# Kernel tuning notes

Hardware: AMD Instinct MI355X
Metric: run time of the kernel (lower is better)

Reference implementation:

```python
import jax, jax.numpy as jnp
import numpy as np

N, D, H, DH, FF, NE, NNZ = 4096, 128, 2, 64, 256, 2048, 65536
EPS = 1e-5

def layer_norm(x, g, b):
    m = jnp.mean(x, axis=-1, keepdims=True)
    v = jnp.var(x, axis=-1, keepdims=True)
    return (x - m) / jnp.sqrt(v + EPS) * g + b

def setup_inputs() -> dict:
    key = jax.random.key(0)
    ks = jax.random.split(key, 24)
    s = 0.05
    node_idx = jax.random.randint(ks[1], (NNZ,), 0, N)
    he_idx = jax.random.randint(ks[2], (NNZ,), 0, NE)
    return {
        "x": jax.random.normal(ks[0], (N, D), dtype=jnp.float32),
        "edge": jnp.stack([node_idx, he_idx]).astype(jnp.int64),
        "Wq": jax.random.normal(ks[3], (D, D)) * s, "bq": jnp.zeros((D,)),
        "Wk": jax.random.normal(ks[4], (D, D)) * s, "bk": jnp.zeros((D,)),
        "Wv": jax.random.normal(ks[5], (D, D)) * s, "bv": jnp.zeros((D,)),
        "Wo": jax.random.normal(ks[6], (D, D)) * s, "bo": jnp.zeros((D,)),
        "g_ln1": jnp.ones((D,)), "b_ln1": jnp.zeros((D,)),
        "W1": jax.random.normal(ks[7], (D, FF)) * s, "bf1": jnp.zeros((FF,)),
        "W2": jax.random.normal(ks[8], (FF, D)) * s, "bf2": jnp.zeros((D,)),
        "g_ln2": jnp.ones((D,)), "b_ln2": jnp.zeros((D,)),
        "Wh": jax.random.normal(ks[9], (D, D)) * s, "bh": jnp.zeros((D,)),
    }

def reference(x, edge, Wq, bq, Wk, bk, Wv, bv, Wo, bo, g_ln1, b_ln1,
              W1, bf1, W2, bf2, g_ln2, b_ln2, Wh, bh):
    # dropout layers run in eval mode (identity) for a deterministic reference
    def mha_block(h):
        q = (h @ Wq + bq).reshape(N, H, DH)
        k = (h @ Wk + bk).reshape(N, H, DH)
        v = (h @ Wv + bv).reshape(N, H, DH)
        scores = jnp.einsum('nhd,mhd->hnm', q, k) / jnp.sqrt(jnp.float32(DH))
        attn = jax.nn.softmax(scores, axis=-1)            # [H,N,N]
        o = jnp.einsum('hnm,mhd->nhd', attn, v).reshape(N, D)
        return layer_norm(h + o @ Wo + bo, g_ln1, b_ln1)

    def ff_block(h):
        z = jax.nn.sigmoid(h @ W1 + bf1)
        return layer_norm(h + z @ W2 + bf2, g_ln2, b_ln2)

    h = ff_block(mha_block(x))
    h = ff_block(mha_block(h))

    # HypergraphConv: out = D^{-1} H B^{-1} H^T (X Theta) + bias
    node_idx = edge[0]
    he_idx = edge[1]
    xt = h @ Wh                                            # [N,D]
    ones = jnp.ones((NNZ,), dtype=xt.dtype)
    Bdeg = jax.ops.segment_sum(ones, he_idx, num_segments=NE)
    Binv = jnp.where(Bdeg > 0, 1.0 / Bdeg, 0.0)
    Ddeg = jax.ops.segment_sum(ones, node_idx, num_segments=N)
    Dinv = jnp.where(Ddeg > 0, 1.0 / Ddeg, 0.0)
    e = jax.ops.segment_sum(xt[node_idx], he_idx, num_segments=NE) * Binv[:, None]
    out = jax.ops.segment_sum(e[he_idx], node_idx, num_segments=N) * Dinv[:, None] + bh
    return jax.nn.relu(out)
```

## Files before the change

### kernel.cpp

```cpp
#include <hip/hip_runtime.h>
#include <hip/hip_bf16.h>
#include <cstddef>

#define N_NODES 4096
#define DIM     128
#define NHEAD   2
#define DHEAD   64
#define FFDIM   256
#define NEDGE   2048
#define NNZ_E   65536
#define NSPLIT  8

typedef __attribute__((ext_vector_type(8))) short bf16x8;
typedef __attribute__((ext_vector_type(4))) float f32x4;
typedef unsigned short u16;

__device__ __forceinline__ u16 f2b(float f) {
    unsigned u = __float_as_uint(f);
    return (u16)((u + 0x7FFFu + ((u >> 16) & 1u)) >> 16);
}
__device__ __forceinline__ float b2f_bits(u16 h) {
    return __uint_as_float(((unsigned)h) << 16);
}

__global__ void prep(const float* __restrict__ x, float* __restrict__ h,
                     u16* __restrict__ hh, u16* __restrict__ hl,
                     const float* W0, const float* W1, const float* W2,
                     const float* W3, const float* W4, const float* W5,
                     const float* W6,
                     u16* P0, u16* P1, u16* P2, u16* P3, u16* P4, u16* P5, u16* P6,
                     int* __restrict__ cnt) {
    const int bx = blockIdx.x;
    if (bx < 2048) {
        int i = bx * 256 + threadIdx.x;
        float f = x[i];
        h[i] = f;
        u16 hi = f2b(f);
        hh[i] = hi;
        hl[i] = f2b(f - b2f_bits(hi));
        return;
    }
    if (bx >= 2944) {
        int i = (bx - 2944) * 256 + threadIdx.x;
        if (i < NEDGE + N_NODES) cnt[i] = 0;
        return;
    }
    const int p = bx - 2048;
    const int sel = p >> 7;
    const float* W; u16* P; int K, NC;
    switch (sel) {
        case 0: W = W0; P = P0; K = 128; NC = 128; break;
        case 1: W = W1; P = P1; K = 128; NC = 128; break;
        case 2: W = W2; P = P2; K = 128; NC = 128; break;
        case 3: W = W3; P = P3; K = 128; NC = 128; break;
        case 4: W = W4; P = P4; K = 128; NC = 128; break;
        case 5: W = W5; P = P5; K = 128; NC = 256; break;
        default: W = W6; P = P6; K = 256; NC = 128; break;
    }
    int i = (p & 127) * 256 + threadIdx.x;
    if (i < K * NC) {
        int k = i / NC, n = i % NC;
        float f = W[i];
        u16 hb = f2b(f);
        size_t o = ((size_t)(k >> 3) * NC + n) * 8 + (k & 7);
        P[o] = hb;
        P[(size_t)K * NC + o] = f2b(f - b2f_bits(hb));
    }
}

template<int K, int NC>
__global__ __launch_bounds__(256) void gemm_mfma(const u16* __restrict__ Ah,
                                                 const u16* __restrict__ Al,
                                                 const u16* __restrict__ Wp,
                                                 float* __restrict__ C0) {
    const int tid = threadIdx.x, w = tid >> 6, lane = tid & 63;
    const int qi = lane & 15, gi = lane >> 4;
    const int row0 = blockIdx.x * 64 + w * 16;
    const int col0 = blockIdx.y * 32;
    const u16* Wlo = Wp + (size_t)K * NC;

    f32x4 acc[2];
    acc[0] = (f32x4){0.f, 0.f, 0.f, 0.f};
    acc[1] = (f32x4){0.f, 0.f, 0.f, 0.f};

#pragma unroll 4
    for (int kc = 0; kc < K / 32; ++kc) {
        const int k0 = kc * 32;
        const size_t ao = (size_t)(row0 + qi) * K + k0 + gi * 8;
        bf16x8 ah = *(const bf16x8*)(Ah + ao);
        bf16x8 al = *(const bf16x8*)(Al + ao);
#pragma unroll
        for (int c = 0; c < 2; ++c) {
            const size_t wo = ((size_t)(k0 / 8 + gi) * NC + col0 + c * 16 + qi) * 8;
            bf16x8 wh = *(const bf16x8*)(Wp + wo);
            bf16x8 wl = *(const bf16x8*)(Wlo + wo);
            acc[c] = __builtin_amdgcn_mfma_f32_16x16x32_bf16(ah, wh, acc[c], 0, 0, 0);
            acc[c] = __builtin_amdgcn_mfma_f32_16x16x32_bf16(al, wh, acc[c], 0, 0, 0);
            acc[c] = __builtin_amdgcn_mfma_f32_16x16x32_bf16(ah, wl, acc[c], 0, 0, 0);
        }
    }

#pragma unroll
    for (int c = 0; c < 2; ++c) {
        const int col = col0 + c * 16 + qi;
#pragma unroll
        for (int r = 0; r < 4; ++r) {
            const int grow = row0 + gi * 4 + r;
            C0[(size_t)grow * NC + col] = acc[c][r];
        }
    }
}

__global__ __launch_bounds__(256) void qkv_mfma(const u16* __restrict__ Ah,
                                                const u16* __restrict__ Al,
                                                const u16* __restrict__ Wq,
                                                const u16* __restrict__ Wk,
                                                const u16* __restrict__ Wv,
                                                const float* __restrict__ bq,
                                                const float* __restrict__ bk,
                                                const float* __restrict__ bv,
                                                u16* __restrict__ qb,
                                                u16* __restrict__ kb,
                                                u16* __restrict__ vtb) {
    const int K = 128, NC = 128;
    const int tid = threadIdx.x, w = tid >> 6, lane = tid & 63;
    const int qi = lane & 15, gi = lane >> 4;
    const int row0 = blockIdx.x * 64 + w * 16;
    const int sel = blockIdx.y >> 2;
    const int col0 = (blockIdx.y & 3) * 32;
    const u16* Wp = (sel == 0) ? Wq : (sel == 1) ? Wk : Wv;
    const float* bias = (sel == 0) ? bq : (sel == 1) ? bk : bv;
    const u16* Wlo = Wp + (size_t)K * NC;

    f32x4 acc[2];
    acc[0] = (f32x4){0.f, 0.f, 0.f, 0.f};
    acc[1] = (f32x4){0.f, 0.f, 0.f, 0.f};

#pragma unroll 4
    for (int kc = 0; kc < K / 32; ++kc) {
        const int k0 = kc * 32;
        const size_t ao = (size_t)(row0 + qi) * K + k0 + gi * 8;
        bf16x8 ah = *(const bf16x8*)(Ah + ao);
        bf16x8 al = *(const bf16x8*)(Al + ao);
#pragma unroll
        for (int c = 0; c < 2; ++c) {
            const size_t wo = ((size_t)(k0 / 8 + gi) * NC + col0 + c * 16 + qi) * 8;
            bf16x8 wh = *(const bf16x8*)(Wp + wo);
            bf16x8 wl = *(const bf16x8*)(Wlo + wo);
            acc[c] = __builtin_amdgcn_mfma_f32_16x16x32_bf16(ah, wh, acc[c], 0, 0, 0);
            acc[c] = __builtin_amdgcn_mfma_f32_16x16x32_bf16(al, wh, acc[c], 0, 0, 0);
            acc[c] = __builtin_amdgcn_mfma_f32_16x16x32_bf16(ah, wl, acc[c], 0, 0, 0);
        }
    }

#pragma unroll
    for (int c = 0; c < 2; ++c) {
        const int col = col0 + c * 16 + qi;
        const int hh = col >> 6, d = col & 63;
        float bv_ = bias[col];
        if (sel < 2) {
            u16* dst = (sel == 0) ? qb : kb;
#pragma unroll
            for (int r = 0; r < 4; ++r) {
                const int grow = row0 + gi * 4 + r;
                dst[((size_t)hh * N_NODES + grow) * 64 + d] = f2b(acc[c][r] + bv_);
            }
        } else {
            const int grow0 = row0 + gi * 4;
            ushort4 pw;
            pw.x = f2b(acc[c][0] + bv_);
            pw.y = f2b(acc[c][1] + bv_);
            pw.z = f2b(acc[c][2] + bv_);
            pw.w = f2b(acc[c][3] + bv_);
            *(ushort4*)&vtb[((size_t)hh * 64 + d) * N_NODES + grow0] = pw;
        }
    }
}

#define ROWP 72
__global__ __launch_bounds__(256) void attn_mfma(const u16* __restrict__ qb,
                                                 const u16* __restrict__ kb,
                                                 const u16* __restrict__ vtb,
                                                 float* __restrict__ op,
                                                 float* __restrict__ mlm,
                                                 float* __restrict__ mll) {
    __shared__ __align__(16) u16 k_s[64 * ROWP];
    __shared__ __align__(16) u16 vt_s[64 * ROWP];
    __shared__ __align__(16) u16 p_s[4][16 * ROWP];
    const int h = blockIdx.y;
    const int s = blockIdx.z;
    const int row0 = blockIdx.x * 64;
    const int tid = threadIdx.x;
    const int w = tid >> 6, lane = tid & 63;
    const int qi = lane & 15, gi = lane >> 4;
    const float CE = 0.18033688011f;

    const u16* qrow = qb + ((size_t)h * N_NODES + row0 + w * 16 + qi) * 64 + gi * 8;
    bf16x8 qf0 = *(const bf16x8*)qrow;
    bf16x8 qf1 = *(const bf16x8*)(qrow + 32);

    f32x4 oc[4];
#pragma unroll
    for (int i = 0; i < 4; ++i) oc[i] = (f32x4){0.f, 0.f, 0.f, 0.f};
    float m_run = -INFINITY, l_run = 0.f;

    const u16* kbh = kb + (size_t)h * N_NODES * 64;
    const u16* vth = vtb + (size_t)h * 64 * N_NODES;

    for (int kt = s * (N_NODES / 64 / NSPLIT); kt < (s + 1) * (N_NODES / 64 / NSPLIT); ++kt) {
        const u16* ksrc = kbh + kt * 64 * 64;
#pragma unroll
        for (int i = 0; i < 2; ++i) {
            int c = tid + i * 256;
            int r = c >> 3, ss = c & 7;
            *(uint4*)&k_s[r * ROWP + ss * 8]  = *(const uint4*)(ksrc + c * 8);
            *(uint4*)&vt_s[r * ROWP + ss * 8] = *(const uint4*)(vth + (size_t)r * N_NODES + kt * 64 + ss * 8);
        }
        __syncthreads();

        f32x4 sc[4];
#pragma unroll
        for (int t = 0; t < 4; ++t) {
            const u16* krow = &k_s[(t * 16 + qi) * ROWP + gi * 8];
            bf16x8 ka0 = *(const bf16x8*)krow;
            bf16x8 ka1 = *(const bf16x8*)(krow + 32);
            f32x4 z = (f32x4){0.f, 0.f, 0.f, 0.f};
            z = __builtin_amdgcn_mfma_f32_16x16x32_bf16(ka0, qf0, z, 0, 0, 0);
            sc[t] = __builtin_amdgcn_mfma_f32_16x16x32_bf16(ka1, qf1, z, 0, 0, 0);
        }

        float smax = -INFINITY;
#pragma unroll
        for (int t = 0; t < 4; ++t)
            smax = fmaxf(smax, fmaxf(fmaxf(sc[t][0], sc[t][1]), fmaxf(sc[t][2], sc[t][3])));
        smax = fmaxf(smax, __shfl_xor(smax, 16));
        smax = fmaxf(smax, __shfl_xor(smax, 32));
        float mn = fmaxf(m_run, smax);
        float alpha = exp2f((m_run - mn) * CE);
        m_run = mn;
        float nb = mn * CE;
        float psum = 0.f;
#pragma unroll
        for (int t = 0; t < 4; ++t) {
            ushort4 pw;
            float p0 = exp2f(fmaf(sc[t][0], CE, -nb)); psum += p0; pw.x = f2b(p0);
            float p1 = exp2f(fmaf(sc[t][1], CE, -nb)); psum += p1; pw.y = f2b(p1);
            float p2 = exp2f(fmaf(sc[t][2], CE, -nb)); psum += p2; pw.z = f2b(p2);
            float p3 = exp2f(fmaf(sc[t][3], CE, -nb)); psum += p3; pw.w = f2b(p3);
            *(ushort4*)&p_s[w][qi * ROWP + t * 16 + gi * 4] = pw;
        }
        psum += __shfl_xor(psum, 16);
        psum += __shfl_xor(psum, 32);
        l_run = l_run * alpha + psum;

        float a0 = __shfl(alpha, gi * 4 + 0);
        float a1 = __shfl(alpha, gi * 4 + 1);
        float a2 = __shfl(alpha, gi * 4 + 2);
        float a3 = __shfl(alpha, gi * 4 + 3);
#pragma unroll
        for (int d = 0; d < 4; ++d) {
            oc[d][0] *= a0; oc[d][1] *= a1; oc[d][2] *= a2; oc[d][3] *= a3;
        }

        const u16* prow = &p_s[w][qi * ROWP];
        bf16x8 pa0 = *(const bf16x8*)(prow + gi * 8);
        bf16x8 pa1 = *(const bf16x8*)(prow + 32 + gi * 8);
#pragma unroll
        for (int d = 0; d < 4; ++d) {
            const u16* vrow = &vt_s[(d * 16 + qi) * ROWP + gi * 8];
            bf16x8 vb0 = *(const bf16x8*)vrow;
            bf16x8 vb1 = *(const bf16x8*)(vrow + 32);
            oc[d] = __builtin_amdgcn_mfma_f32_16x16x32_bf16(pa0, vb0, oc[d], 0, 0, 0);
            oc[d] = __builtin_amdgcn_mfma_f32_16x16x32_bf16(pa1, vb1, oc[d], 0, 0, 0);
        }
        __syncthreads();
    }

    float* opd = op + (size_t)s * N_NODES * 128;
#pragma unroll
    for (int d = 0; d < 4; ++d) {
        size_t cb = h * 64 + d * 16 + qi;
        opd[(size_t)(row0 + w * 16 + gi * 4 + 0) * 128 + cb] = oc[d][0];
        opd[(size_t)(row0 + w * 16 + gi * 4 + 1) * 128 + cb] = oc[d][1];
        opd[(size_t)(row0 + w * 16 + gi * 4 + 2) * 128 + cb] = oc[d][2];
        opd[(size_t)(row0 + w * 16 + gi * 4 + 3) * 128 + cb] = oc[d][3];
    }
    if (gi == 0) {
        size_t mi = (size_t)s * NHEAD * N_NODES + (size_t)h * N_NODES + row0 + w * 16 + qi;
        mlm[mi] = m_run;
        mll[mi] = l_run;
    }
}

#define ROWA 136
#define ROWZ 264
#define ROWH 132
template<int DO_QKV>
__global__ __launch_bounds__(256) void mega_layer(
        const float* __restrict__ op, const float* __restrict__ mlm,
        const float* __restrict__ mll,
        const u16* __restrict__ wp_o, const float* __restrict__ bo,
        float* __restrict__ h,
        const float* __restrict__ g1, const float* __restrict__ b1,
        const u16* __restrict__ wp_1, const float* __restrict__ bf1,
        const u16* __restrict__ wp_2, const float* __restrict__ bf2,
        const float* __restrict__ g2, const float* __restrict__ b2,
        const u16* __restrict__ wp_q, const u16* __restrict__ wp_k,
        const u16* __restrict__ wp_v,
        const float* __restrict__ bq, const float* __restrict__ bk,
        const float* __restrict__ bv,
        u16* __restrict__ qb, u16* __restrict__ kb, u16* __restrict__ vtb) {
    __shared__ __align__(16) u16 zbuf[16 * ROWZ * 2];
    __shared__ __align__(16) u16 hp_hi[16 * ROWA];
    __shared__ __align__(16) u16 hp_lo[16 * ROWA];
    __shared__ float hln[16 * ROWH];
    __shared__ float ws_s[NSPLIT][32];
    __shared__ float Linv_s[32];
    __shared__ float wsum[4][16], wsq[4][16];
    const float CE = 0.18033688011f;
    const int tid = threadIdx.x, w = tid >> 6, lane = tid & 63;
    const int qi = lane & 15, gi = lane >> 4;
    const int row0 = blockIdx.x * 16;
    u16* a_hi = zbuf;
    u16* a_lo = zbuf + 16 * ROWA;
    u16* z_hi = zbuf;
    u16* z_lo = zbuf + 16 * ROWZ;

    if (tid < 32) {
        int r = tid >> 1, hd = tid & 1;
        size_t mb = (size_t)hd * N_NODES + row0 + r;
        float m[NSPLIT], l[NSPLIT], mx = -INFINITY;
#pragma unroll
        for (int s = 0; s < NSPLIT; ++s) {
            m[s] = mlm[mb + (size_t)s * NHEAD * N_NODES];
            l[s] = mll[mb + (size_t)s * NHEAD * N_NODES];
            mx = fmaxf(mx, m[s]);
        }
        float L = 0.f;
#pragma unroll
        for (int s = 0; s < NSPLIT; ++s) {
            float ws = exp2f((m[s] - mx) * CE);
            ws_s[s][tid] = ws;
            L += ws * l[s];
        }
        Linv_s[tid] = 1.f / L;
    }
    __syncthreads();

    for (int e = tid; e < 16 * 128; e += 256) {
        int r = e >> 7, c = e & 127, hd = c >> 6;
        size_t idx = (size_t)(row0 + r) * 128 + c;
        float O = 0.f;
#pragma unroll
        for (int s = 0; s < NSPLIT; ++s)
            O += ws_s[s][r * 2 + hd] * op[(size_t)s * N_NODES * 128 + idx];
        float v = O * Linv_s[r * 2 + hd];
        u16 hi = f2b(v);
        a_hi[r * ROWA + c] = hi;
        a_lo[r * ROWA + c] = f2b(v - b2f_bits(hi));
    }
    __syncthreads();

    {
        const u16* Wlo = wp_o + (size_t)128 * 128;
        f32x4 acc[2];
        acc[0] = (f32x4){0.f, 0.f, 0.f, 0.f};
        acc[1] = (f32x4){0.f, 0.f, 0.f, 0.f};
        const int col0 = w * 32;
#pragma unroll
        for (int kc = 0; kc < 4; ++kc) {
            const int k0 = kc * 32;
            bf16x8 ah = *(const bf16x8*)&a_hi[qi * ROWA + k0 + gi * 8];
            bf16x8 al = *(const bf16x8*)&a_lo[qi * ROWA + k0 + gi * 8];
#pragma unroll
            for (int c = 0; c < 2; ++c) {
                const size_t wo = ((size_t)(k0 / 8 + gi) * 128 + col0 + c * 16 + qi) * 8;
                bf16x8 wh = *(const bf16x8*)(wp_o + wo);
                bf16x8 wl = *(const bf16x8*)(Wlo + wo);
                acc[c] = __builtin_amdgcn_mfma_f32_16x16x32_bf16(ah, wh, acc[c], 0, 0, 0);
                acc[c] = __builtin_amdgcn_mfma_f32_16x16x32_bf16(al, wh, acc[c], 0, 0, 0);
                acc[c] = __builtin_amdgcn_mfma_f32_16x16x32_bf16(ah, wl, acc[c], 0, 0, 0);
            }
        }
        float y[2][4], rs[4], rq[4];
#pragma unroll
        for (int r = 0; r < 4; ++r) { rs[r] = 0.f; rq[r] = 0.f; }
#pragma unroll
        for (int c = 0; c < 2; ++c) {
            const int col = col0 + c * 16 + qi;
            float bv = bo[col];
#pragma unroll
            for (int r = 0; r < 4; ++r) {
                float v = acc[c][r] + bv + h[(size_t)(row0 + gi * 4 + r) * 128 + col];
                y[c][r] = v;
                rs[r] += v; rq[r] += v * v;
            }
        }
#pragma unroll
        for (int r = 0; r < 4; ++r)
            for (int msk = 1; msk < 16; msk <<= 1) {
                rs[r] += __shfl_xor(rs[r], msk);
                rq[r] += __shfl_xor(rq[r], msk);
            }
        if (qi == 0) {
#pragma unroll
            for (int r = 0; r < 4; ++r) { wsum[w][gi * 4 + r] = rs[r]; wsq[w][gi * 4 + r] = rq[r]; }
        }
        __syncthreads();
#pragma unroll
        for (int r = 0; r < 4; ++r) {
            const int lr = gi * 4 + r;
            float ts = wsum[0][lr] + wsum[1][lr] + wsum[2][lr] + wsum[3][lr];
            float tq = wsq[0][lr] + wsq[1][lr] + wsq[2][lr] + wsq[3][lr];
            float mean = ts * (1.f / 128.f);
            float var  = tq * (1.f / 128.f) - mean * mean;
            float rstd = rsqrtf(var + 1e-5f);
#pragma unroll
            for (int c = 0; c < 2; ++c) {
                const int col = col0 + c * 16 + qi;
                float yn = (y[c][r] - mean) * rstd * g1[col] + b1[col];
                hln[lr * ROWH + col] = yn;
                u16 hi = f2b(yn);
                hp_hi[lr * ROWA + col] = hi;
                hp_lo[lr * ROWA + col] = f2b(yn - b2f_bits(hi));
            }
        }
    }
    __syncthreads();

    {
        const u16* W1lo = wp_1 + (size_t)128 * 256;
        f32x4 acc1[4];
#pragma unroll
        for (int t = 0; t < 4; ++t) acc1[t] = (f32x4){0.f, 0.f, 0.f, 0.f};
#pragma unroll
        for (int kc = 0; kc < 4; ++kc) {
            const int k0 = kc * 32;
            bf16x8 ah = *(const bf16x8*)&hp_hi[qi * ROWA + k0 + gi * 8];
            bf16x8 al = *(const bf16x8*)&hp_lo[qi * ROWA + k0 + gi * 8];
#pragma unroll
            for (int t = 0; t < 4; ++t) {
                const size_t wo = ((size_t)(k0 / 8 + gi) * 256 + w * 64 + t * 16 + qi) * 8;
                bf16x8 wh = *(const bf16x8*)(wp_1 + wo);
                bf16x8 wl = *(const bf16x8*)(W1lo + wo);
                acc1[t] = __builtin_amdgcn_mfma_f32_16x16x32_bf16(ah, wh, acc1[t], 0, 0, 0);
                acc1[t] = __builtin_amdgcn_mfma_f32_16x16x32_bf16(al, wh, acc1[t], 0, 0, 0);
                acc1[t] = __builtin_amdgcn_mfma_f32_16x16x32_bf16(ah, wl, acc1[t], 0, 0, 0);
            }
        }
        __syncthreads();
#pragma unroll
        for (int t = 0; t < 4; ++t) {
            const int col = w * 64 + t * 16 + qi;
            float bv = bf1[col];
#pragma unroll
            for (int r = 0; r < 4; ++r) {
                float v = acc1[t][r] + bv;
                v = 1.f / (1.f + __expf(-v));
                u16 hi = f2b(v);
                const int zr = gi * 4 + r;
                z_hi[zr * ROWZ + col] = hi;
                z_lo[zr * ROWZ + col] = f2b(v - b2f_bits(hi));
            }
        }
    }
    __syncthreads();

    {
        const u16* W2lo = wp_2 + (size_t)256 * 128;
        f32x4 acc[2];
        acc[0] = (f32x4){0.f, 0.f, 0.f, 0.f};
        acc[1] = (f32x4){0.f, 0.f, 0.f, 0.f};
        const int col0 = w * 32;
#pragma unroll
        for (int kc = 0; kc < 8; ++kc) {
            const int k0 = kc * 32;
            bf16x8 ah = *(const bf16x8*)&z_hi[qi * ROWZ + k0 + gi * 8];
            bf16x8 al = *(const bf16x8*)&z_lo[qi * ROWZ + k0 + gi * 8];
#pragma unroll
            for (int c = 0; c < 2; ++c) {
                const size_t wo = ((size_t)(k0 / 8 + gi) * 128 + col0 + c * 16 + qi) * 8;
                bf16x8 wh = *(const bf16x8*)(wp_2 + wo);
                bf16x8 wl = *(const bf16x8*)(W2lo + wo);
                acc[c] = __builtin_amdgcn_mfma_f32_16x16x32_bf16(ah, wh, acc[c], 0, 0, 0);
                acc[c] = __builtin_amdgcn_mfma_f32_16x16x32_bf16(al, wh, acc[c], 0, 0, 0);
                acc[c] = __builtin_amdgcn_mfma_f32_16x16x32_bf16(ah, wl, acc[c], 0, 0, 0);
            }
        }
        float y[2][4], rs[4], rq[4];
#pragma unroll
        for (int r = 0; r < 4; ++r) { rs[r] = 0.f; rq[r] = 0.f; }
#pragma unroll
        for (int c = 0; c < 2; ++c) {
            const int col = col0 + c * 16 + qi;
            float bv = bf2[col];
#pragma unroll
            for (int r = 0; r < 4; ++r) {
                float v = acc[c][r] + bv + hln[(gi * 4 + r) * ROWH + col];
                y[c][r] = v;
                rs[r] += v; rq[r] += v * v;
            }
        }
#pragma unroll
        for (int r = 0; r < 4; ++r)
            for (int msk = 1; msk < 16; msk <<= 1) {
                rs[r] += __shfl_xor(rs[r], msk);
                rq[r] += __shfl_xor(rq[r], msk);
            }
        if (qi == 0) {
#pragma unroll
            for (int r = 0; r < 4; ++r) { wsum[w][gi * 4 + r] = rs[r]; wsq[w][gi * 4 + r] = rq[r]; }
        }
        __syncthreads();
#pragma unroll
        for (int r = 0; r < 4; ++r) {
            const int lr = gi * 4 + r;
            float ts = wsum[0][lr] + wsum[1][lr] + wsum[2][lr] + wsum[3][lr];
            float tq = wsq[0][lr] + wsq[1][lr] + wsq[2][lr] + wsq[3][lr];
            float mean = ts * (1.f / 128.f);
            float var  = tq * (1.f / 128.f) - mean * mean;
            float rstd = rsqrtf(var + 1e-5f);
#pragma unroll
            for (int c = 0; c < 2; ++c) {
                const int col = col0 + c * 16 + qi;
                float yn = (y[c][r] - mean) * rstd * g2[col] + b2[col];
                h[(size_t)(row0 + lr) * 128 + col] = yn;
                if (DO_QKV) {
                    u16 hi = f2b(yn);
                    hp_hi[lr * ROWA + col] = hi;
                    hp_lo[lr * ROWA + col] = f2b(yn - b2f_bits(hi));
                }
            }
        }
    }

    if (DO_QKV) {
        __syncthreads();
        const int col0 = w * 32;
#pragma unroll
        for (int sel = 0; sel < 3; ++sel) {
            const u16* Wp = (sel == 0) ? wp_q : (sel == 1) ? wp_k : wp_v;
            const float* bias = (sel == 0) ? bq : (sel == 1) ? bk : bv;
            const u16* Wlo = Wp + (size_t)128 * 128;
            f32x4 acc[2];
            acc[0] = (f32x4){0.f, 0.f, 0.f, 0.f};
            acc[1] = (f32x4){0.f, 0.f, 0.f, 0.f};
#pragma unroll
            for (int kc = 0; kc < 4; ++kc) {
                const int k0 = kc * 32;
                bf16x8 ah = *(const bf16x8*)&hp_hi[qi * ROWA + k0 + gi * 8];
                bf16x8 al = *(const bf16x8*)&hp_lo[qi * ROWA + k0 + gi * 8];
#pragma unroll
                for (int c = 0; c < 2; ++c) {
                    const size_t wo = ((size_t)(k0 / 8 + gi) * 128 + col0 + c * 16 + qi) * 8;
                    bf16x8 wh = *(const bf16x8*)(Wp + wo);
                    bf16x8 wl = *(const bf16x8*)(Wlo + wo);
                    acc[c] = __builtin_amdgcn_mfma_f32_16x16x32_bf16(ah, wh, acc[c], 0, 0, 0);
                    acc[c] = __builtin_amdgcn_mfma_f32_16x16x32_bf16(al, wh, acc[c], 0, 0, 0);
                    acc[c] = __builtin_amdgcn_mfma_f32_16x16x32_bf16(ah, wl, acc[c], 0, 0, 0);
                }
            }
#pragma unroll
            for (int c = 0; c < 2; ++c) {
                const int col = col0 + c * 16 + qi;
                const int hh = col >> 6, d = col & 63;
                float bv_ = bias[col];
                if (sel < 2) {
                    u16* dst = (sel == 0) ? qb : kb;
#pragma unroll
                    for (int r = 0; r < 4; ++r) {
                        const int grow = row0 + gi * 4 + r;
                        dst[((size_t)hh * N_NODES + grow) * 64 + d] = f2b(acc[c][r] + bv_);
                    }
                } else {
                    const int grow0 = row0 + gi * 4;
                    ushort4 pw;
                    pw.x = f2b(acc[c][0] + bv_);
                    pw.y = f2b(acc[c][1] + bv_);
                    pw.z = f2b(acc[c][2] + bv_);
                    pw.w = f2b(acc[c][3] + bv_);
                    *(ushort4*)&vtb[((size_t)hh * 64 + d) * N_NODES + grow0] = pw;
                }
            }
        }
    }
}

__global__ void hist_kernel(const int* __restrict__ edge_raw,
                            int* __restrict__ nidx, int* __restrict__ hidx,
                            int* __restrict__ cnt_e, int* __restrict__ cnt_n) {
    __shared__ int is64_s;
    if (threadIdx.x < 64) {
        int v = edge_raw[2 * threadIdx.x + 1];
        unsigned long long bal = __ballot(v != 0);
        if (threadIdx.x == 0) is64_s = (bal == 0ull) ? 1 : 0;
    }
    __syncthreads();
    const int is64 = is64_s;
    int i = blockIdx.x * 256 + threadIdx.x;
    if (i < NNZ_E) {
        int ni = (is64 ? edge_raw[2 * i]             : edge_raw[i])         & (N_NODES - 1);
        int he = (is64 ? edge_raw[2 * NNZ_E + 2 * i] : edge_raw[NNZ_E + i]) & (NEDGE - 1);
        nidx[i] = ni;
        hidx[i] = he;
        atomicAdd(&cnt_n[ni], 1);
        atomicAdd(&cnt_e[he], 1);
    }
}

__global__ __launch_bounds__(1024) void scan_only(const int* __restrict__ cnt_e,
                                                  const int* __restrict__ cnt_n,
                                                  int* __restrict__ off_e,
                                                  int* __restrict__ off_n,
                                                  int* __restrict__ cur_e,
                                                  int* __restrict__ cur_n) {
    __shared__ int s[N_NODES];
    const int he_side = (blockIdx.x == 0);
    const int n = he_side ? NEDGE : N_NODES;
    const int* cnt = he_side ? cnt_e : cnt_n;
    int* off = he_side ? off_e : off_n;
    int* cur = he_side ? cur_e : cur_n;
    for (int i = threadIdx.x; i < n; i += 1024) s[i] = cnt[i];
    __syncthreads();
    for (int st = 1; st < n; st <<= 1) {
        int v[4]; int nj = 0;
        for (int i = threadIdx.x; i < n; i += 1024) v[nj++] = (i >= st) ? s[i - st] : 0;
        __syncthreads();
        nj = 0;
        for (int i = threadIdx.x; i < n; i += 1024) s[i] += v[nj++];
        __syncthreads();
    }
    for (int i = threadIdx.x; i < n; i += 1024) { off[i + 1] = s[i]; cur[i] = 0; }
    if (threadIdx.x == 0) off[0] = 0;
}

__global__ void fill_csr(const int* __restrict__ nidx, const int* __restrict__ hidx,
                         const int* __restrict__ off_e, const int* __restrict__ off_n,
                         int* __restrict__ cur_e, int* __restrict__ cur_n,
                         int* __restrict__ csr_e, int* __restrict__ csr_n) {
    int i = blockIdx.x * 256 + threadIdx.x;
    if (i < NNZ_E) {
        int ni = nidx[i], he = hidx[i];
        int p = atomicAdd(&cur_e[he], 1);
        csr_e[off_e[he] + p] = ni;
        int q = atomicAdd(&cur_n[ni], 1);
        csr_n[off_n[ni] + q] = he;
    }
}

__global__ __launch_bounds__(128) void gather_e(const int* __restrict__ off_e,
                                                const int* __restrict__ csr_e,
                                                const float* __restrict__ h,
                                                u16* __restrict__ ehi,
                                                u16* __restrict__ elo) {
    __shared__ int ms[128];
    const int he = blockIdx.x, d = threadIdx.x;
    const int beg = off_e[he], end = off_e[he + 1];
    float acc = 0.f;
    for (int c = beg; c < end; c += 128) {
        int nl = min(128, end - c);
        if (d < nl) ms[d] = csr_e[c + d];
        __syncthreads();
        for (int j = 0; j < nl; ++j) acc += h[(size_t)ms[j] * 128 + d];
        __syncthreads();
    }
    float binv = (end > beg) ? 1.f / (float)(end - beg) : 0.f;
    float v = acc * binv;
    u16 hi = f2b(v);
    ehi[(size_t)he * 128 + d] = hi;
    elo[(size_t)he * 128 + d] = f2b(v - b2f_bits(hi));
}

__global__ __launch_bounds__(128) void gather_n(const int* __restrict__ off_n,
                                                const int* __restrict__ csr_n,
                                                const float* __restrict__ e_sc,
                                                const float* __restrict__ bh,
                                                float* __restrict__ out) {
    __shared__ int ms[128];
    const int nn = blockIdx.x, d = threadIdx.x;
    const int beg = off_n[nn], end = off_n[nn + 1];
    float acc = 0.f;
    for (int c = beg; c < end; c += 128) {
        int nl = min(128, end - c);
        if (d < nl) ms[d] = csr_n[c + d];
        __syncthreads();
        for (int j = 0; j < nl; ++j) acc += e_sc[(size_t)ms[j] * 128 + d];
        __syncthreads();
    }
    float dinv = (end > beg) ? 1.f / (float)(end - beg) : 0.f;
    float v = acc * dinv + bh[d];
    out[(size_t)nn * 128 + d] = v > 0.f ? v : 0.f;
}

extern "C" void kernel_launch(void* const* d_in, const int* in_sizes, int n_in,
                              void* d_out, int out_size, void* d_ws, size_t ws_size,
                              hipStream_t stream) {
    (void)in_sizes; (void)n_in; (void)out_size; (void)ws_size;
    const float* x    = (const float*)d_in[0];
    const int*   edge = (const int*)  d_in[1];
    const float* Wq = (const float*)d_in[2];  const float* bq  = (const float*)d_in[3];
    const float* Wk = (const float*)d_in[4];  const float* bk  = (const float*)d_in[5];
    const float* Wv = (const float*)d_in[6];  const float* bv  = (const float*)d_in[7];
    const float* Wo = (const float*)d_in[8];  const float* bo  = (const float*)d_in[9];
    const float* g1 = (const float*)d_in[10]; const float* b1  = (const float*)d_in[11];
    const float* W1 = (const float*)d_in[12]; const float* bf1 = (const float*)d_in[13];
    const float* W2 = (const float*)d_in[14]; const float* bf2 = (const float*)d_in[15];
    const float* g2 = (const float*)d_in[16]; const float* b2  = (const float*)d_in[17];
    const float* Wh = (const float*)d_in[18]; const float* bh  = (const float*)d_in[19];
    float* out = (float*)d_out;

    float* B = (float*)d_ws;
    float* h    = B;
    u16*   h_hi = (u16*)(B + 524288);
    u16*   h_lo = (u16*)(B + 786432);
    u16*   qb   = (u16*)(B + 1048576);
    u16*   kb   = (u16*)(B + 1310720);
    u16*   vtb  = (u16*)(B + 1835008);
    float* op   = B + 2097152;
    float* mlm  = B + 6291456;
    float* mll  = B + 6356992;
    u16*   e_hi = (u16*)(B + 6946816);
    u16*   e_lo = (u16*)(B + 7077888);
    float* e_sc = B + 7208960;
    u16*   wp_q = (u16*)(B + 8519680);
    u16*   wp_k = (u16*)(B + 8536064);
    u16*   wp_v = (u16*)(B + 8552448);
    u16*   wp_o = (u16*)(B + 8568832);
    u16*   wp_h = (u16*)(B + 8585216);
    u16*   wp_1 = (u16*)(B + 8601600);
    u16*   wp_2 = (u16*)(B + 8634368);
    int*   cur_e = (int*)(B + 9328640);
    int*   cur_n = (int*)(B + 9330688);
    int*   off_e = (int*)(B + 9334784);
    int*   off_n = (int*)(B + 9336840);
    int*   csr_e = (int*)(B + 9340944);
    int*   csr_n = (int*)(B + 9406480);
    int*   cnt_e = (int*)(B + 9472016);
    int*   cnt_n = (int*)(B + 9474064);
    int*   nidx  = (int*)(B + 9478160);
    int*   hidx  = (int*)(B + 9543696);

    prep<<<2969, 256, 0, stream>>>(x, h, h_hi, h_lo,
                                   Wq, Wk, Wv, Wo, Wh, W1, W2,
                                   wp_q, wp_k, wp_v, wp_o, wp_h, wp_1, wp_2, cnt_e);

    qkv_mfma<<<dim3(64, 12), 256, 0, stream>>>(h_hi, h_lo, wp_q, wp_k, wp_v,
                                               bq, bk, bv, qb, kb, vtb);
    attn_mfma<<<dim3(N_NODES / 64, NHEAD, NSPLIT), 256, 0, stream>>>(qb, kb, vtb, op, mlm, mll);
    mega_layer<1><<<N_NODES / 16, 256, 0, stream>>>(op, mlm, mll, wp_o, bo, h, g1, b1,
                                                    wp_1, bf1, wp_2, bf2, g2, b2,
                                                    wp_q, wp_k, wp_v, bq, bk, bv,
                                                    qb, kb, vtb);
    attn_mfma<<<dim3(N_NODES / 64, NHEAD, NSPLIT), 256, 0, stream>>>(qb, kb, vtb, op, mlm, mll);
    mega_layer<0><<<N_NODES / 16, 256, 0, stream>>>(op, mlm, mll, wp_o, bo, h, g1, b1,
                                                    wp_1, bf1, wp_2, bf2, g2, b2,
                                                    nullptr, nullptr, nullptr,
                                                    nullptr, nullptr, nullptr,
                                                    nullptr, nullptr, nullptr);

    hist_kernel<<<NNZ_E / 256, 256, 0, stream>>>(edge, nidx, hidx, cnt_e, cnt_n);
    scan_only<<<2, 1024, 0, stream>>>(cnt_e, cnt_n, off_e, off_n, cur_e, cur_n);
    fill_csr<<<NNZ_E / 256, 256, 0, stream>>>(nidx, hidx, off_e, off_n, cur_e, cur_n, csr_e, csr_n);
    gather_e<<<NEDGE, 128, 0, stream>>>(off_e, csr_e, h, e_hi, e_lo);
    gemm_mfma<128, 128><<<dim3(NEDGE / 64, 4), 256, 0, stream>>>(e_hi, e_lo, wp_h, e_sc);
    gather_n<<<N_NODES, 128, 0, stream>>>(off_n, csr_n, e_sc, bh, out);
}
```

Baseline: 252.7 us.

## Fuse Wh GEMM into final layer, merge histogram into prep, lazy softmax rescale

The Wh projection now runs inside the last mega_layer instead of as a separate gemm after gathering, so gather_e sums pre-projected rows. The edge histogram moves into the prep kernel, with counters cleared by a memset. Attention skips the online-softmax rescale when the new max stays within a threshold of the running max. Packed bf16 conversion instructions replace manual rounding, and the gather loops are unrolled to four accumulators. Together these remove two launches and some per-tile exp and multiply work, but they change rounding order, and the softmax threshold relies on exp2 not overflowing.

```diff
diff --git a/kernel.cpp b/kernel.cpp
--- a/kernel.cpp
+++ b/kernel.cpp
@@ -22,6 +22,11 @@
 __device__ __forceinline__ float b2f_bits(u16 h) {
     return __uint_as_float(((unsigned)h) << 16);
 }
+__device__ __forceinline__ unsigned cvtpk(float a, float b) {
+    unsigned r;
+    asm("v_cvt_pk_bf16_f32 %0, %1, %2" : "=v"(r) : "v"(a), "v"(b));
+    return r;
+}
 
 __global__ void prep(const float* __restrict__ x, float* __restrict__ h,
                      u16* __restrict__ hh, u16* __restrict__ hl,
@@ -29,7 +34,9 @@
                      const float* W3, const float* W4, const float* W5,
                      const float* W6,
                      u16* P0, u16* P1, u16* P2, u16* P3, u16* P4, u16* P5, u16* P6,
-                     int* __restrict__ cnt) {
+                     const int* __restrict__ edge_raw,
+                     int* __restrict__ nidx, int* __restrict__ hidx,
+                     int* __restrict__ cnt_e, int* __restrict__ cnt_n) {
     const int bx = blockIdx.x;
     if (bx < 2048) {
         int i = bx * 256 + threadIdx.x;
@@ -41,8 +48,23 @@
         return;
     }
     if (bx >= 2944) {
+        __shared__ int is64_s;
+        if (threadIdx.x < 64) {
+            int v = edge_raw[2 * threadIdx.x + 1];
+            unsigned long long bal = __ballot(v != 0);
+            if (threadIdx.x == 0) is64_s = (bal == 0ull) ? 1 : 0;
+        }
+        __syncthreads();
+        const int is64 = is64_s;
         int i = (bx - 2944) * 256 + threadIdx.x;
-        if (i < NEDGE + N_NODES) cnt[i] = 0;
+        if (i < NNZ_E) {
+            int ni = (is64 ? edge_raw[2 * i]             : edge_raw[i])         & (N_NODES - 1);
+            int he = (is64 ? edge_raw[2 * NNZ_E + 2 * i] : edge_raw[NNZ_E + i]) & (NEDGE - 1);
+            nidx[i] = ni;
+            hidx[i] = he;
+            atomicAdd(&cnt_n[ni], 1);
+            atomicAdd(&cnt_e[he], 1);
+        }
         return;
     }
     const int p = bx - 2048;
@@ -65,49 +87,6 @@
         size_t o = ((size_t)(k >> 3) * NC + n) * 8 + (k & 7);
         P[o] = hb;
         P[(size_t)K * NC + o] = f2b(f - b2f_bits(hb));
-    }
-}
-
-template<int K, int NC>
-__global__ __launch_bounds__(256) void gemm_mfma(const u16* __restrict__ Ah,
-                                                 const u16* __restrict__ Al,
-                                                 const u16* __restrict__ Wp,
-                                                 float* __restrict__ C0) {
-    const int tid = threadIdx.x, w = tid >> 6, lane = tid & 63;
-    const int qi = lane & 15, gi = lane >> 4;
-    const int row0 = blockIdx.x * 64 + w * 16;
-    const int col0 = blockIdx.y * 32;
-    const u16* Wlo = Wp + (size_t)K * NC;
-
-    f32x4 acc[2];
-    acc[0] = (f32x4){0.f, 0.f, 0.f, 0.f};
-    acc[1] = (f32x4){0.f, 0.f, 0.f, 0.f};
-
-#pragma unroll 4
-    for (int kc = 0; kc < K / 32; ++kc) {
-        const int k0 = kc * 32;
-        const size_t ao = (size_t)(row0 + qi) * K + k0 + gi * 8;
-        bf16x8 ah = *(const bf16x8*)(Ah + ao);
-        bf16x8 al = *(const bf16x8*)(Al + ao);
-#pragma unroll
-        for (int c = 0; c < 2; ++c) {
-            const size_t wo = ((size_t)(k0 / 8 + gi) * NC + col0 + c * 16 + qi) * 8;
-            bf16x8 wh = *(const bf16x8*)(Wp + wo);
-            bf16x8 wl = *(const bf16x8*)(Wlo + wo);
-            acc[c] = __builtin_amdgcn_mfma_f32_16x16x32_bf16(ah, wh, acc[c], 0, 0, 0);
-            acc[c] = __builtin_amdgcn_mfma_f32_16x16x32_bf16(al, wh, acc[c], 0, 0, 0);
-            acc[c] = __builtin_amdgcn_mfma_f32_16x16x32_bf16(ah, wl, acc[c], 0, 0, 0);
-        }
-    }
-
-#pragma unroll
-    for (int c = 0; c < 2; ++c) {
-        const int col = col0 + c * 16 + qi;
-#pragma unroll
-        for (int r = 0; r < 4; ++r) {
-            const int grow = row0 + gi * 4 + r;
-            C0[(size_t)grow * NC + col] = acc[c][r];
-        }
     }
 }
 
@@ -167,12 +146,10 @@
             }
         } else {
             const int grow0 = row0 + gi * 4;
-            ushort4 pw;
-            pw.x = f2b(acc[c][0] + bv_);
-            pw.y = f2b(acc[c][1] + bv_);
-            pw.z = f2b(acc[c][2] + bv_);
-            pw.w = f2b(acc[c][3] + bv_);
-            *(ushort4*)&vtb[((size_t)hh * 64 + d) * N_NODES + grow0] = pw;
+            uint2 pw;
+            pw.x = cvtpk(acc[c][0] + bv_, acc[c][1] + bv_);
+            pw.y = cvtpk(acc[c][2] + bv_, acc[c][3] + bv_);
+            *(uint2*)&vtb[((size_t)hh * 64 + d) * N_NODES + grow0] = pw;
         }
     }
 }
@@ -194,6 +171,7 @@
     const int w = tid >> 6, lane = tid & 63;
     const int qi = lane & 15, gi = lane >> 4;
     const float CE = 0.18033688011f;
+    const float THR = 44.36f;
 
     const u16* qrow = qb + ((size_t)h * N_NODES + row0 + w * 16 + qi) * 64 + gi * 8;
     bf16x8 qf0 = *(const bf16x8*)qrow;
@@ -235,31 +213,43 @@
             smax = fmaxf(smax, fmaxf(fmaxf(sc[t][0], sc[t][1]), fmaxf(sc[t][2], sc[t][3])));
         smax = fmaxf(smax, __shfl_xor(smax, 16));
         smax = fmaxf(smax, __shfl_xor(smax, 32));
-        float mn = fmaxf(m_run, smax);
-        float alpha = exp2f((m_run - mn) * CE);
-        m_run = mn;
-        float nb = mn * CE;
+
+        const bool renew = !__all(smax <= m_run + THR);
+        float alpha;
+        if (renew) {
+            float mn = fmaxf(m_run, smax);
+            alpha = exp2f((m_run - mn) * CE);
+            m_run = mn;
+        }
+        float nb = m_run * CE;
         float psum = 0.f;
 #pragma unroll
         for (int t = 0; t < 4; ++t) {
-            ushort4 pw;
-            float p0 = exp2f(fmaf(sc[t][0], CE, -nb)); psum += p0; pw.x = f2b(p0);
-            float p1 = exp2f(fmaf(sc[t][1], CE, -nb)); psum += p1; pw.y = f2b(p1);
-            float p2 = exp2f(fmaf(sc[t][2], CE, -nb)); psum += p2; pw.z = f2b(p2);
-            float p3 = exp2f(fmaf(sc[t][3], CE, -nb)); psum += p3; pw.w = f2b(p3);
-            *(ushort4*)&p_s[w][qi * ROWP + t * 16 + gi * 4] = pw;
+            float p0 = exp2f(fmaf(sc[t][0], CE, -nb));
+            float p1 = exp2f(fmaf(sc[t][1], CE, -nb));
+            float p2 = exp2f(fmaf(sc[t][2], CE, -nb));
+            float p3 = exp2f(fmaf(sc[t][3], CE, -nb));
+            psum += (p0 + p1) + (p2 + p3);
+            uint2 pw;
+            pw.x = cvtpk(p0, p1);
+            pw.y = cvtpk(p2, p3);
+            *(uint2*)&p_s[w][qi * ROWP + t * 16 + gi * 4] = pw;
         }
         psum += __shfl_xor(psum, 16);
         psum += __shfl_xor(psum, 32);
-        l_run = l_run * alpha + psum;
-
-        float a0 = __shfl(alpha, gi * 4 + 0);
-        float a1 = __shfl(alpha, gi * 4 + 1);
-        float a2 = __shfl(alpha, gi * 4 + 2);
-        float a3 = __shfl(alpha, gi * 4 + 3);
-#pragma unroll
-        for (int d = 0; d < 4; ++d) {
-            oc[d][0] *= a0; oc[d][1] *= a1; oc[d][2] *= a2; oc[d][3] *= a3;
+
+        if (renew) {
+            float a0 = __shfl(alpha, gi * 4 + 0);
+            float a1 = __shfl(alpha, gi * 4 + 1);
+            float a2 = __shfl(alpha, gi * 4 + 2);
+            float a3 = __shfl(alpha, gi * 4 + 3);
+#pragma unroll
+            for (int d = 0; d < 4; ++d) {
+                oc[d][0] *= a0; oc[d][1] *= a1; oc[d][2] *= a2; oc[d][3] *= a3;
+            }
+            l_run = l_run * alpha + psum;
+        } else {
+            l_run += psum;
         }
 
         const u16* prow = &p_s[w][qi * ROWP];
@@ -309,7 +299,8 @@
         const u16* __restrict__ wp_v,
         const float* __restrict__ bq, const float* __restrict__ bk,
         const float* __restrict__ bv,
-        u16* __restrict__ qb, u16* __restrict__ kb, u16* __restrict__ vtb) {
+        u16* __restrict__ qb, u16* __restrict__ kb, u16* __restrict__ vtb,
+        const u16* __restrict__ wp_h, float* __restrict__ xt) {
     __shared__ __align__(16) u16 zbuf[16 * ROWZ * 2];
     __shared__ __align__(16) u16 hp_hi[16 * ROWA];
     __shared__ __align__(16) u16 hp_lo[16 * ROWA];
@@ -524,12 +515,10 @@
             for (int c = 0; c < 2; ++c) {
                 const int col = col0 + c * 16 + qi;
                 float yn = (y[c][r] - mean) * rstd * g2[col] + b2[col];
-                h[(size_t)(row0 + lr) * 128 + col] = yn;
-                if (DO_QKV) {
-                    u16 hi = f2b(yn);
-                    hp_hi[lr * ROWA + col] = hi;
-                    hp_lo[lr * ROWA + col] = f2b(yn - b2f_bits(hi));
-                }
+                if (DO_QKV) h[(size_t)(row0 + lr) * 128 + col] = yn;
+                u16 hi = f2b(yn);
+                hp_hi[lr * ROWA + col] = hi;
+                hp_lo[lr * ROWA + col] = f2b(yn - b2f_bits(hi));
             }
         }
     }
@@ -574,37 +563,42 @@
                     }
                 } else {
                     const int grow0 = row0 + gi * 4;
-                    ushort4 pw;
-                    pw.x = f2b(acc[c][0] + bv_);
-                    pw.y = f2b(acc[c][1] + bv_);
-                    pw.z = f2b(acc[c][2] + bv_);
-                    pw.w = f2b(acc[c][3] + bv_);
-                    *(ushort4*)&vtb[((size_t)hh * 64 + d) * N_NODES + grow0] = pw;
+                    uint2 pw;
+                    pw.x = cvtpk(acc[c][0] + bv_, acc[c][1] + bv_);
+                    pw.y = cvtpk(acc[c][2] + bv_, acc[c][3] + bv_);
+                    *(uint2*)&vtb[((size_t)hh * 64 + d) * N_NODES + grow0] = pw;
                 }
             }
         }
-    }
-}
-
-__global__ void hist_kernel(const int* __restrict__ edge_raw,
-                            int* __restrict__ nidx, int* __restrict__ hidx,
-                            int* __restrict__ cnt_e, int* __restrict__ cnt_n) {
-    __shared__ int is64_s;
-    if (threadIdx.x < 64) {
-        int v = edge_raw[2 * threadIdx.x + 1];
-        unsigned long long bal = __ballot(v != 0);
-        if (threadIdx.x == 0) is64_s = (bal == 0ull) ? 1 : 0;
-    }
-    __syncthreads();
-    const int is64 = is64_s;
-    int i = blockIdx.x * 256 + threadIdx.x;
-    if (i < NNZ_E) {
-        int ni = (is64 ? edge_raw[2 * i]             : edge_raw[i])         & (N_NODES - 1);
-        int he = (is64 ? edge_raw[2 * NNZ_E + 2 * i] : edge_raw[NNZ_E + i]) & (NEDGE - 1);
-        nidx[i] = ni;
-        hidx[i] = he;
-        atomicAdd(&cnt_n[ni], 1);
-        atomicAdd(&cnt_e[he], 1);
+    } else {
+        __syncthreads();
+        const u16* Wlo = wp_h + (size_t)128 * 128;
+        f32x4 acc[2];
+        acc[0] = (f32x4){0.f, 0.f, 0.f, 0.f};
+        acc[1] = (f32x4){0.f, 0.f, 0.f, 0.f};
+        const int col0 = w * 32;
+#pragma unroll
+        for (int kc = 0; kc < 4; ++kc) {
+            const int k0 = kc * 32;
+            bf16x8 ah = *(const bf16x8*)&hp_hi[qi * ROWA + k0 + gi * 8];
+            bf16x8 al = *(const bf16x8*)&hp_lo[qi * ROWA + k0 + gi * 8];
+#pragma unroll
+            for (int c = 0; c < 2; ++c) {
+                const size_t wo = ((size_t)(k0 / 8 + gi) * 128 + col0 + c * 16 + qi) * 8;
+                bf16x8 wh = *(const bf16x8*)(wp_h + wo);
+                bf16x8 wl = *(const bf16x8*)(Wlo + wo);
+                acc[c] = __builtin_amdgcn_mfma_f32_16x16x32_bf16(ah, wh, acc[c], 0, 0, 0);
+                acc[c] = __builtin_amdgcn_mfma_f32_16x16x32_bf16(al, wh, acc[c], 0, 0, 0);
+                acc[c] = __builtin_amdgcn_mfma_f32_16x16x32_bf16(ah, wl, acc[c], 0, 0, 0);
+            }
+        }
+#pragma unroll
+        for (int c = 0; c < 2; ++c) {
+            const int col = col0 + c * 16 + qi;
+#pragma unroll
+            for (int r = 0; r < 4; ++r)
+                xt[(size_t)(row0 + gi * 4 + r) * 128 + col] = acc[c][r];
+        }
     }
 }
 
@@ -650,25 +644,28 @@
 
 __global__ __launch_bounds__(128) void gather_e(const int* __restrict__ off_e,
                                                 const int* __restrict__ csr_e,
-                                                const float* __restrict__ h,
-                                                u16* __restrict__ ehi,
-                                                u16* __restrict__ elo) {
+                                                const float* __restrict__ xt,
+                                                float* __restrict__ e_sc) {
     __shared__ int ms[128];
     const int he = blockIdx.x, d = threadIdx.x;
     const int beg = off_e[he], end = off_e[he + 1];
-    float acc = 0.f;
+    float a0 = 0.f, a1 = 0.f, a2 = 0.f, a3 = 0.f;
     for (int c = beg; c < end; c += 128) {
         int nl = min(128, end - c);
         if (d < nl) ms[d] = csr_e[c + d];
         __syncthreads();
-        for (int j = 0; j < nl; ++j) acc += h[(size_t)ms[j] * 128 + d];
+        int j = 0;
+        for (; j + 3 < nl; j += 4) {
+            a0 += xt[(size_t)ms[j]     * 128 + d];
+            a1 += xt[(size_t)ms[j + 1] * 128 + d];
+            a2 += xt[(size_t)ms[j + 2] * 128 + d];
+            a3 += xt[(size_t)ms[j + 3] * 128 + d];
+        }
+        for (; j < nl; ++j) a0 += xt[(size_t)ms[j] * 128 + d];
         __syncthreads();
     }
     float binv = (end > beg) ? 1.f / (float)(end - beg) : 0.f;
-    float v = acc * binv;
-    u16 hi = f2b(v);
-    ehi[(size_t)he * 128 + d] = hi;
-    elo[(size_t)he * 128 + d] = f2b(v - b2f_bits(hi));
+    e_sc[(size_t)he * 128 + d] = ((a0 + a1) + (a2 + a3)) * binv;
 }
 
 __global__ __launch_bounds__(128) void gather_n(const int* __restrict__ off_n,
@@ -679,16 +676,23 @@
     __shared__ int ms[128];
     const int nn = blockIdx.x, d = threadIdx.x;
     const int beg = off_n[nn], end = off_n[nn + 1];
-    float acc = 0.f;
+    float a0 = 0.f, a1 = 0.f, a2 = 0.f, a3 = 0.f;
     for (int c = beg; c < end; c += 128) {
         int nl = min(128, end - c);
         if (d < nl) ms[d] = csr_n[c + d];
         __syncthreads();
-        for (int j = 0; j < nl; ++j) acc += e_sc[(size_t)ms[j] * 128 + d];
+        int j = 0;
+        for (; j + 3 < nl; j += 4) {
+            a0 += e_sc[(size_t)ms[j]     * 128 + d];
+            a1 += e_sc[(size_t)ms[j + 1] * 128 + d];
+            a2 += e_sc[(size_t)ms[j + 2] * 128 + d];
+            a3 += e_sc[(size_t)ms[j + 3] * 128 + d];
+        }
+        for (; j < nl; ++j) a0 += e_sc[(size_t)ms[j] * 128 + d];
         __syncthreads();
     }
     float dinv = (end > beg) ? 1.f / (float)(end - beg) : 0.f;
-    float v = acc * dinv + bh[d];
+    float v = ((a0 + a1) + (a2 + a3)) * dinv + bh[d];
     out[(size_t)nn * 128 + d] = v > 0.f ? v : 0.f;
 }
 
@@ -719,9 +723,8 @@
     float* op   = B + 2097152;
     float* mlm  = B + 6291456;
     float* mll  = B + 6356992;
-    u16*   e_hi = (u16*)(B + 6946816);
-    u16*   e_lo = (u16*)(B + 7077888);
-    float* e_sc = B + 7208960;
+    float* xt   = B + 6946816;
+    float* e_sc = B + 7471104;
     u16*   wp_q = (u16*)(B + 8519680);
     u16*   wp_k = (u16*)(B + 8536064);
     u16*   wp_v = (u16*)(B + 8552448);
@@ -740,9 +743,12 @@
     int*   nidx  = (int*)(B + 9478160);
     int*   hidx  = (int*)(B + 9543696);
 
-    prep<<<2969, 256, 0, stream>>>(x, h, h_hi, h_lo,
+    hipMemsetAsync(cnt_e, 0, (NEDGE + N_NODES) * sizeof(int), stream);
+
+    prep<<<3200, 256, 0, stream>>>(x, h, h_hi, h_lo,
                                    Wq, Wk, Wv, Wo, Wh, W1, W2,
-                                   wp_q, wp_k, wp_v, wp_o, wp_h, wp_1, wp_2, cnt_e);
+                                   wp_q, wp_k, wp_v, wp_o, wp_h, wp_1, wp_2,
+                                   edge, nidx, hidx, cnt_e, cnt_n);
 
     qkv_mfma<<<dim3(64, 12), 256, 0, stream>>>(h_hi, h_lo, wp_q, wp_k, wp_v,
                                                bq, bk, bv, qb, kb, vtb);
@@ -750,18 +756,17 @@
     mega_layer<1><<<N_NODES / 16, 256, 0, stream>>>(op, mlm, mll, wp_o, bo, h, g1, b1,
                                                     wp_1, bf1, wp_2, bf2, g2, b2,
                                                     wp_q, wp_k, wp_v, bq, bk, bv,
-                                                    qb, kb, vtb);
+                                                    qb, kb, vtb, wp_h, xt);
     attn_mfma<<<dim3(N_NODES / 64, NHEAD, NSPLIT), 256, 0, stream>>>(qb, kb, vtb, op, mlm, mll);
     mega_layer<0><<<N_NODES / 16, 256, 0, stream>>>(op, mlm, mll, wp_o, bo, h, g1, b1,
                                                     wp_1, bf1, wp_2, bf2, g2, b2,
                                                     nullptr, nullptr, nullptr,
                                                     nullptr, nullptr, nullptr,
-                                                    nullptr, nullptr, nullptr);
-
-    hist_kernel<<<NNZ_E / 256, 256, 0, stream>>>(edge, nidx, hidx, cnt_e, cnt_n);
+                                                    nullptr, nullptr, nullptr,
+                                                    wp_h, xt);
+
     scan_only<<<2, 1024, 0, stream>>>(cnt_e, cnt_n, off_e, off_n, cur_e, cur_n);
     fill_csr<<<NNZ_E / 256, 256, 0, stream>>>(nidx, hidx, off_e, off_n, cur_e, cur_n, csr_e, csr_n);
-    gather_e<<<NEDGE, 128, 0, stream>>>(off_e, csr_e, h, e_hi, e_lo);
-    gemm_mfma<128, 128><<<dim3(NEDGE / 64, 4), 256, 0, stream>>>(e_hi, e_lo, wp_h, e_sc);
+    gather_e<<<NEDGE, 128, 0, stream>>>(off_e, csr_e, xt, e_sc);
     gather_n<<<N_NODES, 128, 0, stream>>>(off_n, csr_n, e_sc, bh, out);
 }
```

New measurement: 255.6 us. No clear change (+1.1%).
